# Kernel tuning notes

Measured on AMD Instinct MI355X. Metric: run time of the kernel, lower is better.

## Reference

```python
import jax, jax.numpy as jnp
import numpy as np

B, R, NM, H, P1, G1, RC1, LAT = 16384, 360, 200, 256, 512, 256, 256, 128


def _linear_params(k, out_f, in_f):
    s = 1.0 / np.sqrt(in_f)
    kw, kb = jax.random.split(k)
    W = jax.random.uniform(kw, (out_f, in_f), minval=-s, maxval=s, dtype=jnp.float32)
    b = jax.random.uniform(kb, (out_f,), minval=-s, maxval=s, dtype=jnp.float32)
    return W, b


def setup_inputs() -> dict:
    key = jax.random.key(0)
    ks = jax.random.split(key, 14)
    x_window = jax.random.normal(ks[0], (B, 3, R), dtype=jnp.float32)
    modes = jax.random.normal(ks[1], (R, NM), dtype=jnp.float32)
    mode_coeff = jax.random.normal(ks[2], (B, NM), dtype=jnp.float32)
    W1, b1 = _linear_params(ks[3], H, 3 * R)      # surrogate layer 1
    W2, b2 = _linear_params(ks[4], H, H)          # surrogate layer 2
    W3, b3 = _linear_params(ks[5], R, H)          # surrogate layer 3
    Wp1, bp1 = _linear_params(ks[6], P1, R * R)   # npi_proj
    Wp2, bp2 = _linear_params(ks[7], LAT, P1)
    Wg1, bg1 = _linear_params(ks[8], G1, NM)      # geo_proj
    Wg2, bg2 = _linear_params(ks[9], LAT, G1)
    Wr1, br1 = _linear_params(ks[10], RC1, LAT)   # recon
    Wr2, br2 = _linear_params(ks[11], R, RC1)
    return dict(x_window=x_window, modes=modes, mode_coeff=mode_coeff,
                W1=W1, b1=b1, W2=W2, b2=b2, W3=W3, b3=b3,
                Wp1=Wp1, bp1=bp1, Wp2=Wp2, bp2=bp2,
                Wg1=Wg1, bg1=bg1, Wg2=Wg2, bg2=bg2,
                Wr1=Wr1, br1=br1, Wr2=Wr2, br2=br2)


def reference(x_window, modes, mode_coeff,
              W1, b1, W2, b2, W3, b3,
              Wp1, bp1, Wp2, bp2,
              Wg1, bg1, Wg2, bg2,
              Wr1, br1, Wr2, br2):
    Bs = x_window.shape[0]
    Rr = W3.shape[0]
    # ---- NPI surrogate forward (needed for ReLU masks) ----
    z = x_window.reshape(Bs, 3 * Rr)                       # (B, 3R)
    h1 = z @ W1.T + b1                                     # (B, H)
    m1 = (h1 > 0).astype(z.dtype)
    h2 = (h1 * m1) @ W2.T + b2                             # (B, H)
    m2 = (h2 > 0).astype(z.dtype)
    # ---- EC: exact batch-mean Jacobian of the ReLU MLP w.r.t last timestep ----
    # mean_b [ W3 diag(m2_b) W2 diag(m1_b) W1_last ] = W3 @ (W2 * (m2^T m1 / B)) @ W1[:, -R:]
    G = (m2.T @ m1) / Bs                                   # (H, H)
    ec = W3 @ ((W2 * G) @ W1[:, -Rr:])                     # (R, R); row j = dy_j/dx
    ec = jax.lax.stop_gradient(ec)                         # create_graph=False in original
    # ---- projections ----
    ec_flat = ec.reshape(1, Rr * Rr)
    z_npi1 = jax.nn.relu(ec_flat @ Wp1.T + bp1) @ Wp2.T + bp2   # (1, LAT)
    z_npi = jnp.tile(z_npi1, (Bs, 1))                           # (B, LAT)
    z_geo = jax.nn.relu(mode_coeff @ Wg1.T + bg1) @ Wg2.T + bg2  # (B, LAT)
    zsum = z_npi + z_geo
    zn = zsum / jnp.maximum(jnp.linalg.norm(zsum, axis=-1, keepdims=True), 1e-12)
    recon = jax.nn.relu(zn @ Wr1.T + br1) @ Wr2.T + br2          # (B, R)
    return (z_npi, z_geo, zn, ec, recon)
```

## Files before the change

kernel.cpp:

```cpp
#include <hip/hip_runtime.h>

typedef __bf16 bf16x8 __attribute__((ext_vector_type(8)));
typedef __bf16 bf16x4 __attribute__((ext_vector_type(4)));
typedef float  f32x4  __attribute__((ext_vector_type(4)));

__device__ __forceinline__ f32x4 mfma_bf16(bf16x8 a, bf16x8 b, f32x4 c) {
  return __builtin_amdgcn_mfma_f32_16x16x32_bf16(a, b, c, 0, 0, 0);
}
__device__ __forceinline__ bf16x8 ldB(const __bf16* Bp, int kt, int NT, int nt,
                                      int lane) {
  return *reinterpret_cast<const bf16x8*>(Bp + (((size_t)kt * NT + nt) * 64 + lane) * 8);
}

__device__ __forceinline__ void gridbar(int* cnt, int target) {
  __syncthreads();
  if (threadIdx.x == 0) {
    __threadfence();
    __hip_atomic_fetch_add(cnt, 1, __ATOMIC_RELEASE, __HIP_MEMORY_SCOPE_AGENT);
    while (__hip_atomic_load(cnt, __ATOMIC_RELAXED, __HIP_MEMORY_SCOPE_AGENT) < target)
      __builtin_amdgcn_s_sleep(4);
    __threadfence();
  }
  __syncthreads();
}

__global__ void pack_all(const float* __restrict__ W1, const float* __restrict__ W2,
                         const float* __restrict__ Wg1, const float* __restrict__ Wg2,
                         const float* __restrict__ Wr1, const float* __restrict__ Wr2,
                         __bf16* __restrict__ W1p, __bf16* __restrict__ W2p,
                         __bf16* __restrict__ Wg1p, __bf16* __restrict__ Wg2p,
                         __bf16* __restrict__ Wr1p, __bf16* __restrict__ Wr2p,
                         float* __restrict__ G, int* __restrict__ cnt) {
  int bx = blockIdx.x;
  int lane = threadIdx.x;
  if (bx >= 1104) {
    if (bx == 1104 && lane < 2) cnt[lane] = 0;
    float4* g = (float4*)G;
    int base = (bx - 1104) * 512 + lane;
#pragma unroll
    for (int i = 0; i < 8; ++i) g[base + i * 64] = make_float4(0.f, 0.f, 0.f, 0.f);
    return;
  }
  const float* W; __bf16* out; int N, K, NT, local;
  if (bx < 544)      { W = W1;  out = W1p;  N = 256; K = 1080; NT = 16; local = bx; }
  else if (bx < 672) { W = W2;  out = W2p;  N = 256; K = 256;  NT = 16; local = bx - 544; }
  else if (bx < 784) { W = Wg1; out = Wg1p; N = 256; K = 200;  NT = 16; local = bx - 672; }
  else if (bx < 848) { W = Wg2; out = Wg2p; N = 128; K = 256;  NT = 8;  local = bx - 784; }
  else if (bx < 912) { W = Wr1; out = Wr1p; N = 256; K = 128;  NT = 16; local = bx - 848; }
  else               { W = Wr2; out = Wr2p; N = 360; K = 256;  NT = 24; local = bx - 912; }
  int nt = local % NT, kt = local / NT;
  int n = nt * 16 + (lane & 15);
  int k0 = kt * 32 + (lane >> 4) * 8;
  bf16x8 v;
#pragma unroll
  for (int e = 0; e < 8; ++e) {
    int k = k0 + e;
    float xv = (n < N && k < K) ? W[(size_t)n * K + k] : 0.f;
    v[e] = (__bf16)xv;
  }
  *reinterpret_cast<bf16x8*>(out + ((size_t)local * 64 + lane) * 8) = v;
}

__global__ __launch_bounds__(512) void h1h2_fused(
    const float* __restrict__ x, const __bf16* __restrict__ W1p,
    const float* __restrict__ b1, const __bf16* __restrict__ W2p,
    const float* __restrict__ b2, __bf16* __restrict__ m1T,
    __bf16* __restrict__ m2T) {
  __shared__ __bf16 Alds[32][68];
  __shared__ __bf16 h1s[32][264];
  int tid = threadIdx.x;
  int lane = tid & 63, wid = tid >> 6;
  int wr = wid >> 2, wc = wid & 3;
  int rowBase = blockIdx.x * 32;
  int sr = tid >> 4, sc = (tid & 15) * 4;
  const float* aSrc = x + (size_t)(rowBase + sr) * 1080;
  f32x4 acc[4] = {};
  float4 c0, c1;
  auto LD = [&](int s, float4& d) {
    int gk = s * 64 + sc;
    d = (gk < 1080) ? *(const float4*)(aSrc + gk) : make_float4(0.f, 0.f, 0.f, 0.f);
  };
  LD(0, c0);
  LD(1, c1);
  for (int s = 0; s < 17; ++s) {
    bf16x4 w4;
    w4[0] = (__bf16)c0.x; w4[1] = (__bf16)c0.y;
    w4[2] = (__bf16)c0.z; w4[3] = (__bf16)c0.w;
    *reinterpret_cast<bf16x4*>(&Alds[sr][sc]) = w4;
    __syncthreads();
    c0 = c1;
    if (s + 2 < 17) LD(s + 2, c1);
    int arow = wr * 16 + (lane & 15);
#pragma unroll
    for (int ks = 0; ks < 2; ++ks) {
      int ak = ks * 32 + (lane >> 4) * 8;
      bf16x8 a0 = *reinterpret_cast<const bf16x8*>(&Alds[arow][ak]);
      int kt = s * 2 + ks;
#pragma unroll
      for (int n = 0; n < 4; ++n) {
        bf16x8 bv = ldB(W1p, kt, 16, wc * 4 + n, lane);
        acc[n] = mfma_bf16(a0, bv, acc[n]);
      }
    }
    __syncthreads();
  }
  int q4 = (lane >> 4) * 4;
#pragma unroll
  for (int n = 0; n < 4; ++n) {
    int col = wc * 64 + n * 16 + (lane & 15);
    float bb = b1[col];
#pragma unroll
    for (int j = 0; j < 4; ++j) {
      int rl = wr * 16 + q4 + j;
      float h = acc[n][j] + bb;
      m1T[(size_t)col * 16384 + rowBase + rl] = (__bf16)(h > 0.f ? 1.f : 0.f);
      h1s[rl][col] = (__bf16)fmaxf(h, 0.f);
    }
  }
  __syncthreads();
  f32x4 acc2[4] = {};
#pragma unroll
  for (int ks = 0; ks < 8; ++ks) {
    int arow = wr * 16 + (lane & 15), ak = ks * 32 + (lane >> 4) * 8;
    bf16x8 a0 = *reinterpret_cast<const bf16x8*>(&h1s[arow][ak]);
#pragma unroll
    for (int n = 0; n < 4; ++n) {
      bf16x8 bv = ldB(W2p, ks, 16, wc * 4 + n, lane);
      acc2[n] = mfma_bf16(a0, bv, acc2[n]);
    }
  }
#pragma unroll
  for (int n = 0; n < 4; ++n) {
    int col = wc * 64 + n * 16 + (lane & 15);
    float bb = b2[col];
#pragma unroll
    for (int j = 0; j < 4; ++j) {
      int rl = wr * 16 + q4 + j;
      float h = acc2[n][j] + bb;
      m2T[(size_t)col * 16384 + rowBase + rl] = (__bf16)(h > 0.f ? 1.f : 0.f);
    }
  }
}

__global__ __launch_bounds__(256) void gemm_masks(
    const __bf16* __restrict__ m2T, const __bf16* __restrict__ m1T,
    float* __restrict__ G) {
  int tid = threadIdx.x;
  int lane = tid & 63, wid = tid >> 6;
  int wr = wid >> 1, wc = wid & 1;
  int ibase = blockIdx.x * 64, jbase = blockIdx.y * 64;
  size_t b0 = (size_t)blockIdx.z * 1024 + (lane >> 4) * 8;
  const __bf16* pa0 = m2T + (size_t)(ibase + wr * 32 + (lane & 15)) * 16384 + b0;
  const __bf16* pa1 = pa0 + (size_t)16 * 16384;
  const __bf16* pb0 = m1T + (size_t)(jbase + wc * 32 + (lane & 15)) * 16384 + b0;
  const __bf16* pb1 = pb0 + (size_t)16 * 16384;
  f32x4 acc[2][2] = {};
#pragma unroll 4
  for (int c = 0; c < 32; ++c) {
    bf16x8 a0 = *reinterpret_cast<const bf16x8*>(pa0 + c * 32);
    bf16x8 a1 = *reinterpret_cast<const bf16x8*>(pa1 + c * 32);
    bf16x8 bv0 = *reinterpret_cast<const bf16x8*>(pb0 + c * 32);
    bf16x8 bv1 = *reinterpret_cast<const bf16x8*>(pb1 + c * 32);
    acc[0][0] = mfma_bf16(a0, bv0, acc[0][0]);
    acc[0][1] = mfma_bf16(a0, bv1, acc[0][1]);
    acc[1][0] = mfma_bf16(a1, bv0, acc[1][0]);
    acc[1][1] = mfma_bf16(a1, bv1, acc[1][1]);
  }
  int q4 = (lane >> 4) * 4;
#pragma unroll
  for (int m = 0; m < 2; ++m)
#pragma unroll
    for (int n = 0; n < 2; ++n)
#pragma unroll
      for (int j = 0; j < 4; ++j) {
        int gi = ibase + wr * 32 + m * 16 + q4 + j;
        int gj = jbase + wc * 32 + n * 16 + (lane & 15);
        atomicAdd(&G[(size_t)gi * 256 + gj], acc[m][n][j] * (1.f / 16384.f));
      }
}

__device__ void small_body2(float (*As)[17], float (*Bs)[65], int t,
                            const float* __restrict__ A, const float* __restrict__ A2,
                            int lda, const float* __restrict__ Bm, int ldb,
                            bool sum4, size_t bStride, float* __restrict__ C,
                            int ldc, int M, int N, int kBeg, int kEnd,
                            int m0, int n0) {
  int tx = t & 15, ty = t >> 4;
  float acc[4][4] = {};
  for (int k0 = kBeg; k0 < kEnd; k0 += 16) {
#pragma unroll
    for (int i = 0; i < 4; ++i) {
      int idx = t * 4 + i;
      int r = idx >> 4, kk = idx & 15;
      int gm = m0 + r, gk = k0 + kk;
      float v = (gm < M) ? A[(size_t)gm * lda + gk] : 0.f;
      if (A2 && gm < M) v *= A2[(size_t)gm * lda + gk];
      As[r][kk] = v;
      int kk2 = idx >> 6, cc = idx & 63;
      int gk2 = k0 + kk2, gn = n0 + cc;
      float bv = 0.f;
      if (gn < N) {
        const float* bp = Bm + (size_t)gk2 * ldb + gn;
        bv = bp[0];
        if (sum4) bv = bv + bp[bStride] + bp[2 * bStride] + bp[3 * bStride];
      }
      Bs[kk2][cc] = bv;
    }
    __syncthreads();
#pragma unroll
    for (int kk = 0; kk < 16; ++kk)
#pragma unroll
      for (int i = 0; i < 4; ++i)
#pragma unroll
        for (int j = 0; j < 4; ++j)
          acc[i][j] += As[ty * 4 + i][kk] * Bs[kk][tx * 4 + j];
    __syncthreads();
  }
#pragma unroll
  for (int i = 0; i < 4; ++i)
#pragma unroll
    for (int j = 0; j < 4; ++j) {
      int gm = m0 + ty * 4 + i, gn = n0 + tx * 4 + j;
      if (gm < M && gn < N) C[(size_t)gm * ldc + gn] = acc[i][j];
    }
}

__global__ __launch_bounds__(256) void small_split(
    const float* __restrict__ W2, const float* __restrict__ G,
    const float* __restrict__ W1, const float* __restrict__ W3,
    float* __restrict__ Tpart, float* __restrict__ ecpart,
    float* __restrict__ o_ec, int* __restrict__ cnt) {
  __shared__ float As[64][17];
  __shared__ float Bs[16][65];
  int t = threadIdx.x, bid = blockIdx.x;
  if (bid < 96) {
    int tile = bid >> 2, kc = bid & 3;
    small_body2(As, Bs, t, W2, G, 256, W1 + 720, 1080, false, 0,
                Tpart + (size_t)kc * 98304, 384, 256, 360,
                kc * 64, kc * 64 + 64, (tile / 6) * 64, (tile % 6) * 64);
  }
  gridbar(cnt, 144);
  {
    int tile = bid >> 2, kc = bid & 3;
    small_body2(As, Bs, t, W3, nullptr, 256, Tpart, 384, true, 98304,
                ecpart + (size_t)kc * 129600, 360, 360, 360,
                kc * 64, kc * 64 + 64, (tile / 6) * 64, (tile % 6) * 64);
  }
  gridbar(cnt, 288);
  {
    int base = bid * 900;
    for (int i = t; i < 900; i += 256) {
      int idx = base + i;
      o_ec[idx] = ecpart[idx] + ecpart[129600 + idx] + ecpart[259200 + idx] +
                  ecpart[388800 + idx];
    }
  }
}

__global__ __launch_bounds__(512) void p_and_g1(
    const float* __restrict__ Wp1, const float* __restrict__ ec,
    float* __restrict__ pPart,
    const float* __restrict__ mc, const __bf16* __restrict__ Wg1p,
    const float* __restrict__ bg1, const __bf16* __restrict__ Wg2p,
    const float* __restrict__ bg2, float* __restrict__ o_zgeo) {
  __shared__ __align__(16) char SM[39424];
  int t = threadIdx.x;
  if (blockIdx.x < 256) {
    int lane = t & 63, w = t >> 6;
    int task = blockIdx.x * 8 + w;
    int row = task >> 2;
    int seg = task & 3;
    const float4* wseg = (const float4*)(Wp1 + (size_t)row * 129600) + seg * 8100;
    const float4* eseg = (const float4*)ec + seg * 8100;
    float s = 0.f;
#pragma unroll 4
    for (int i = lane; i < 8100; i += 64) {
      float4 a = wseg[i], b = eseg[i];
      s += a.x * b.x + a.y * b.y + a.z * b.z + a.w * b.w;
    }
    for (int o = 32; o; o >>= 1) s += __shfl_down(s, o);
    if (lane == 0) pPart[seg * 512 + row] = s;
  } else {
    __bf16 (*Alds)[40] = (__bf16(*)[40])SM;
    __bf16 (*g1S)[264] = (__bf16(*)[264])(SM + 5120);
    int lane = t & 63, wid = t >> 6;
    int wr = wid >> 2, wc = wid & 3;
    int rowBase = (blockIdx.x - 256) * 64;
    int sr = t >> 3, sc = (t & 7) * 4;
    const float* aSrc = mc + (size_t)(rowBase + sr) * 200;
    int q4 = (lane >> 4) * 4;
    f32x4 acc[2][4] = {};
    for (int kt = 0; kt < 7; ++kt) {
      int gk = kt * 32 + sc;
      bf16x4 w4;
      if (gk < 200) {
        float4 v = *(const float4*)(aSrc + gk);
        w4[0] = (__bf16)v.x; w4[1] = (__bf16)v.y;
        w4[2] = (__bf16)v.z; w4[3] = (__bf16)v.w;
      } else {
        w4[0] = w4[1] = w4[2] = w4[3] = (__bf16)0.f;
      }
      *reinterpret_cast<bf16x4*>(&Alds[sr][sc]) = w4;
      __syncthreads();
      int arow = wr * 32 + (lane & 15), ak = (lane >> 4) * 8;
      bf16x8 a0 = *reinterpret_cast<const bf16x8*>(&Alds[arow][ak]);
      bf16x8 a1 = *reinterpret_cast<const bf16x8*>(&Alds[arow + 16][ak]);
#pragma unroll
      for (int n = 0; n < 4; ++n) {
        bf16x8 bv = ldB(Wg1p, kt, 16, wc * 4 + n, lane);
        acc[0][n] = mfma_bf16(a0, bv, acc[0][n]);
        acc[1][n] = mfma_bf16(a1, bv, acc[1][n]);
      }
      __syncthreads();
    }
#pragma unroll
    for (int m = 0; m < 2; ++m)
#pragma unroll
      for (int n = 0; n < 4; ++n) {
        int col = wc * 64 + n * 16 + (lane & 15);
        float bb = bg1[col];
#pragma unroll
        for (int j = 0; j < 4; ++j) {
          int rl = wr * 32 + m * 16 + q4 + j;
          g1S[rl][col] = (__bf16)fmaxf(acc[m][n][j] + bb, 0.f);
        }
      }
    __syncthreads();
    f32x4 acc2[2][2] = {};
#pragma unroll
    for (int ks = 0; ks < 8; ++ks) {
      int arow = wr * 32 + (lane & 15), ak = ks * 32 + (lane >> 4) * 8;
      bf16x8 a0 = *reinterpret_cast<const bf16x8*>(&g1S[arow][ak]);
      bf16x8 a1 = *reinterpret_cast<const bf16x8*>(&g1S[arow + 16][ak]);
#pragma unroll
      for (int n = 0; n < 2; ++n) {
        bf16x8 bv = ldB(Wg2p, ks, 8, wc * 2 + n, lane);
        acc2[0][n] = mfma_bf16(a0, bv, acc2[0][n]);
        acc2[1][n] = mfma_bf16(a1, bv, acc2[1][n]);
      }
    }
#pragma unroll
    for (int m = 0; m < 2; ++m)
#pragma unroll
      for (int n = 0; n < 2; ++n) {
        int col = wc * 32 + n * 16 + (lane & 15);
        float bb = bg2[col];
#pragma unroll
        for (int j = 0; j < 4; ++j) {
          int row = rowBase + wr * 32 + m * 16 + q4 + j;
          o_zgeo[(size_t)row * 128 + col] = acc2[m][n][j] + bb;
        }
      }
  }
}

__global__ void gemv_z(const float* __restrict__ pPart,
                       const float* __restrict__ bp1,
                       const float* __restrict__ Wp2,
                       const float* __restrict__ bp2,
                       float* __restrict__ znpi1) {
  __shared__ __align__(16) float pS[512];
  int j = blockIdx.x;
  int t = threadIdx.x;
#pragma unroll
  for (int r0 = 0; r0 < 512; r0 += 64) {
    int r = r0 + t;
    float v = pPart[r] + pPart[512 + r] + pPart[1024 + r] + pPart[1536 + r];
    pS[r] = fmaxf(v + bp1[r], 0.f);
  }
  __syncthreads();
  const float4* w = (const float4*)(Wp2 + (size_t)j * 512);
  const float4* pp = (const float4*)pS;
  float4 a0 = w[t], b0 = pp[t];
  float4 a1 = w[t + 64], b1 = pp[t + 64];
  float s = a0.x * b0.x + a0.y * b0.y + a0.z * b0.z + a0.w * b0.w +
            a1.x * b1.x + a1.y * b1.y + a1.z * b1.z + a1.w * b1.w;
  for (int o = 32; o; o >>= 1) s += __shfl_down(s, o);
  if (t == 0) znpi1[j] = s + bp2[j];
}

__global__ __launch_bounds__(512) void mega_tail(
    const float* __restrict__ zgeo, const float* __restrict__ znpi1,
    const __bf16* __restrict__ Wr1p, const float* __restrict__ br1,
    const __bf16* __restrict__ Wr2p, const float* __restrict__ br2,
    float* __restrict__ o_znpi, float* __restrict__ o_zn,
    float* __restrict__ o_rec) {
  __shared__ __bf16 r1S[64][264];
  __shared__ __bf16 znS[64][136];
  __shared__ float znpiS[128];
  int tid = threadIdx.x;
  int lane = tid & 63, wid = tid >> 6;
  int wr = wid >> 2, wc = wid & 3;
  int rowBase = blockIdx.x * 64;
  int q4 = (lane >> 4) * 4;
  if (tid < 128) znpiS[tid] = znpi1[tid];
  __syncthreads();
  {
    int rg = tid >> 5;
    int c4 = (tid & 31) * 4;
    float4 zp = make_float4(znpiS[c4], znpiS[c4 + 1], znpiS[c4 + 2], znpiS[c4 + 3]);
#pragma unroll
    for (int ri = 0; ri < 4; ++ri) {
      int rl = rg + ri * 16;
      int row = rowBase + rl;
      float4 zg = *(const float4*)(zgeo + (size_t)row * 128 + c4);
      float4 zs = make_float4(zg.x + zp.x, zg.y + zp.y, zg.z + zp.z, zg.w + zp.w);
      *(float4*)(o_znpi + (size_t)row * 128 + c4) = zp;
      float ss = zs.x * zs.x + zs.y * zs.y + zs.z * zs.z + zs.w * zs.w;
      ss += __shfl_xor(ss, 1);
      ss += __shfl_xor(ss, 2);
      ss += __shfl_xor(ss, 4);
      ss += __shfl_xor(ss, 8);
      ss += __shfl_xor(ss, 16);
      float rn = 1.f / fmaxf(sqrtf(ss), 1e-12f);
      float4 zn = make_float4(zs.x * rn, zs.y * rn, zs.z * rn, zs.w * rn);
      *(float4*)(o_zn + (size_t)row * 128 + c4) = zn;
      bf16x4 znb;
      znb[0] = (__bf16)zn.x; znb[1] = (__bf16)zn.y;
      znb[2] = (__bf16)zn.z; znb[3] = (__bf16)zn.w;
      *reinterpret_cast<bf16x4*>(&znS[rl][c4]) = znb;
    }
  }
  __syncthreads();
  {
    f32x4 acc[2][4] = {};
#pragma unroll
    for (int ks = 0; ks < 4; ++ks) {
      int arow = wr * 32 + (lane & 15), ak = ks * 32 + (lane >> 4) * 8;
      bf16x8 a0 = *reinterpret_cast<const bf16x8*>(&znS[arow][ak]);
      bf16x8 a1 = *reinterpret_cast<const bf16x8*>(&znS[arow + 16][ak]);
#pragma unroll
      for (int n = 0; n < 4; ++n) {
        bf16x8 bv = ldB(Wr1p, ks, 16, wc * 4 + n, lane);
        acc[0][n] = mfma_bf16(a0, bv, acc[0][n]);
        acc[1][n] = mfma_bf16(a1, bv, acc[1][n]);
      }
    }
#pragma unroll
    for (int m = 0; m < 2; ++m)
#pragma unroll
      for (int n = 0; n < 4; ++n) {
        int col = wc * 64 + n * 16 + (lane & 15);
        float bb = br1[col];
#pragma unroll
        for (int j = 0; j < 4; ++j) {
          int rl = wr * 32 + m * 16 + q4 + j;
          r1S[rl][col] = (__bf16)fmaxf(acc[m][n][j] + bb, 0.f);
        }
      }
  }
  __syncthreads();
  {
    f32x4 acc[2][6] = {};
#pragma unroll
    for (int ks = 0; ks < 8; ++ks) {
      int arow = wr * 32 + (lane & 15), ak = ks * 32 + (lane >> 4) * 8;
      bf16x8 a0 = *reinterpret_cast<const bf16x8*>(&r1S[arow][ak]);
      bf16x8 a1 = *reinterpret_cast<const bf16x8*>(&r1S[arow + 16][ak]);
#pragma unroll
      for (int n = 0; n < 6; ++n) {
        bf16x8 bv = ldB(Wr2p, ks, 24, wc * 6 + n, lane);
        acc[0][n] = mfma_bf16(a0, bv, acc[0][n]);
        acc[1][n] = mfma_bf16(a1, bv, acc[1][n]);
      }
    }
#pragma unroll
    for (int m = 0; m < 2; ++m)
#pragma unroll
      for (int n = 0; n < 6; ++n) {
        int col = wc * 96 + n * 16 + (lane & 15);
        if (col < 360) {
          float bb = br2[col];
#pragma unroll
          for (int j = 0; j < 4; ++j) {
            int rl = wr * 32 + m * 16 + q4 + j;
            o_rec[(size_t)(rowBase + rl) * 360 + col] = acc[m][n][j] + bb;
          }
        }
      }
  }
}

extern "C" void kernel_launch(void* const* d_in, const int* in_sizes, int n_in,
                              void* d_out, int out_size, void* d_ws,
                              size_t ws_size, hipStream_t stream) {
  (void)in_sizes; (void)n_in; (void)out_size; (void)ws_size;
  const float* x   = (const float*)d_in[0];
  const float* mc  = (const float*)d_in[2];
  const float* W1  = (const float*)d_in[3];  const float* b1  = (const float*)d_in[4];
  const float* W2  = (const float*)d_in[5];  const float* b2  = (const float*)d_in[6];
  const float* W3  = (const float*)d_in[7];
  const float* Wp1 = (const float*)d_in[9];  const float* bp1 = (const float*)d_in[10];
  const float* Wp2 = (const float*)d_in[11]; const float* bp2 = (const float*)d_in[12];
  const float* Wg1 = (const float*)d_in[13]; const float* bg1 = (const float*)d_in[14];
  const float* Wg2 = (const float*)d_in[15]; const float* bg2 = (const float*)d_in[16];
  const float* Wr1 = (const float*)d_in[17]; const float* br1 = (const float*)d_in[18];
  const float* Wr2 = (const float*)d_in[19]; const float* br2 = (const float*)d_in[20];

  float* out = (float*)d_out;
  float* o_znpi = out;
  float* o_zgeo = out + 2097152;
  float* o_zn   = out + 4194304;
  float* o_ec   = out + 6291456;
  float* o_rec  = out + 6421056;

  char* ws = (char*)d_ws;
  __bf16* m1T    = (__bf16*)(ws + 0);
  __bf16* m2T    = (__bf16*)(ws + 8388608);
  float*  G      = (float*)(ws + 16777216);
  float*  Tpart  = (float*)(ws + 17039360);
  float*  ecpart = (float*)(ws + 18612224);
  float*  pPart  = (float*)(ws + 20686848);
  float*  znpi1  = (float*)(ws + 20695040);
  __bf16* W1p    = (__bf16*)(ws + 20695552);
  __bf16* W2p    = W1p  + (size_t)544 * 512;
  __bf16* Wg1p   = W2p  + (size_t)128 * 512;
  __bf16* Wg2p   = Wg1p + (size_t)112 * 512;
  __bf16* Wr1p   = Wg2p + (size_t)64 * 512;
  __bf16* Wr2p   = Wr1p + (size_t)64 * 512;
  int*    cnt    = (int*)(ws + 22020096);

  pack_all<<<1136, 64, 0, stream>>>(W1, W2, Wg1, Wg2, Wr1, Wr2,
                                    W1p, W2p, Wg1p, Wg2p, Wr1p, Wr2p, G, cnt);
  h1h2_fused<<<512, 512, 0, stream>>>(x, W1p, b1, W2p, b2, m1T, m2T);
  gemm_masks<<<dim3(4, 4, 16), 256, 0, stream>>>(m2T, m1T, G);
  small_split<<<144, 256, 0, stream>>>(W2, G, W1, W3, Tpart, ecpart, o_ec,
                                       cnt);
  p_and_g1<<<512, 512, 0, stream>>>(Wp1, o_ec, pPart, mc, Wg1p, bg1,
                                    Wg2p, bg2, o_zgeo);
  gemv_z<<<128, 64, 0, stream>>>(pPart, bp1, Wp2, bp2, znpi1);
  mega_tail<<<256, 512, 0, stream>>>(o_zgeo, znpi1, Wr1p, br1, Wr2p, br2,
                                     o_znpi, o_zn, o_rec);
}
```

Before: 225.1 us.

## Co-schedule geo projection with mask GEMM, fold z_npi gemv into tail kernel

The geo projection (mode_coeff through Wg1/Wg2) moves out of the Wp1 GEMV kernel and runs in the same launch as the mask Gram GEMM, so independent work overlaps with it. The Wp1 GEMV becomes its own kernel with one row per block and 8 segments per row. The small Wp2 GEMV that produces z_npi is recomputed inside every mega_tail block instead of running as a separate launch. This removes one kernel launch and the dependency stall, at the cost of the Wp2 GEMV being repeated in all 256 tail blocks and half-idle 512-thread blocks in the mask part.

```diff
diff --git a/kernel.cpp b/kernel.cpp
--- a/kernel.cpp
+++ b/kernel.cpp
@@ -34,7 +34,7 @@
   int bx = blockIdx.x;
   int lane = threadIdx.x;
   if (bx >= 1104) {
-    if (bx == 1104 && lane < 2) cnt[lane] = 0;
+    if (bx == 1104 && lane == 0) cnt[0] = 0;
     float4* g = (float4*)G;
     int base = (bx - 1104) * 512 + lane;
 #pragma unroll
@@ -142,41 +142,120 @@
   }
 }
 
-__global__ __launch_bounds__(256) void gemm_masks(
+__global__ __launch_bounds__(512) void masks_g1(
     const __bf16* __restrict__ m2T, const __bf16* __restrict__ m1T,
-    float* __restrict__ G) {
-  int tid = threadIdx.x;
-  int lane = tid & 63, wid = tid >> 6;
-  int wr = wid >> 1, wc = wid & 1;
-  int ibase = blockIdx.x * 64, jbase = blockIdx.y * 64;
-  size_t b0 = (size_t)blockIdx.z * 1024 + (lane >> 4) * 8;
-  const __bf16* pa0 = m2T + (size_t)(ibase + wr * 32 + (lane & 15)) * 16384 + b0;
-  const __bf16* pa1 = pa0 + (size_t)16 * 16384;
-  const __bf16* pb0 = m1T + (size_t)(jbase + wc * 32 + (lane & 15)) * 16384 + b0;
-  const __bf16* pb1 = pb0 + (size_t)16 * 16384;
-  f32x4 acc[2][2] = {};
+    float* __restrict__ G,
+    const float* __restrict__ mc, const __bf16* __restrict__ Wg1p,
+    const float* __restrict__ bg1, const __bf16* __restrict__ Wg2p,
+    const float* __restrict__ bg2, float* __restrict__ o_zgeo) {
+  __shared__ __align__(16) char SM[39424];
+  int tid = threadIdx.x, bid = blockIdx.x;
+  if (bid < 256) {
+    if (tid >= 256) return;
+    int lane = tid & 63, wid = tid >> 6;
+    int wr = wid >> 1, wc = wid & 1;
+    int i = (bid >> 2) & 3, j = bid & 3, z = bid >> 4;
+    int ibase = i * 64, jbase = j * 64;
+    size_t b0 = (size_t)z * 1024 + (lane >> 4) * 8;
+    const __bf16* pa0 = m2T + (size_t)(ibase + wr * 32 + (lane & 15)) * 16384 + b0;
+    const __bf16* pa1 = pa0 + (size_t)16 * 16384;
+    const __bf16* pb0 = m1T + (size_t)(jbase + wc * 32 + (lane & 15)) * 16384 + b0;
+    const __bf16* pb1 = pb0 + (size_t)16 * 16384;
+    f32x4 acc[2][2] = {};
 #pragma unroll 4
-  for (int c = 0; c < 32; ++c) {
-    bf16x8 a0 = *reinterpret_cast<const bf16x8*>(pa0 + c * 32);
-    bf16x8 a1 = *reinterpret_cast<const bf16x8*>(pa1 + c * 32);
-    bf16x8 bv0 = *reinterpret_cast<const bf16x8*>(pb0 + c * 32);
-    bf16x8 bv1 = *reinterpret_cast<const bf16x8*>(pb1 + c * 32);
-    acc[0][0] = mfma_bf16(a0, bv0, acc[0][0]);
-    acc[0][1] = mfma_bf16(a0, bv1, acc[0][1]);
-    acc[1][0] = mfma_bf16(a1, bv0, acc[1][0]);
-    acc[1][1] = mfma_bf16(a1, bv1, acc[1][1]);
-  }
-  int q4 = (lane >> 4) * 4;
-#pragma unroll
-  for (int m = 0; m < 2; ++m)
-#pragma unroll
-    for (int n = 0; n < 2; ++n)
-#pragma unroll
-      for (int j = 0; j < 4; ++j) {
-        int gi = ibase + wr * 32 + m * 16 + q4 + j;
-        int gj = jbase + wc * 32 + n * 16 + (lane & 15);
-        atomicAdd(&G[(size_t)gi * 256 + gj], acc[m][n][j] * (1.f / 16384.f));
-      }
+    for (int c = 0; c < 32; ++c) {
+      bf16x8 a0 = *reinterpret_cast<const bf16x8*>(pa0 + c * 32);
+      bf16x8 a1 = *reinterpret_cast<const bf16x8*>(pa1 + c * 32);
+      bf16x8 bv0 = *reinterpret_cast<const bf16x8*>(pb0 + c * 32);
+      bf16x8 bv1 = *reinterpret_cast<const bf16x8*>(pb1 + c * 32);
+      acc[0][0] = mfma_bf16(a0, bv0, acc[0][0]);
+      acc[0][1] = mfma_bf16(a0, bv1, acc[0][1]);
+      acc[1][0] = mfma_bf16(a1, bv0, acc[1][0]);
+      acc[1][1] = mfma_bf16(a1, bv1, acc[1][1]);
+    }
+    int q4 = (lane >> 4) * 4;
+#pragma unroll
+    for (int m = 0; m < 2; ++m)
+#pragma unroll
+      for (int n = 0; n < 2; ++n)
+#pragma unroll
+        for (int jj = 0; jj < 4; ++jj) {
+          int gi = ibase + wr * 32 + m * 16 + q4 + jj;
+          int gj = jbase + wc * 32 + n * 16 + (lane & 15);
+          atomicAdd(&G[(size_t)gi * 256 + gj], acc[m][n][jj] * (1.f / 16384.f));
+        }
+  } else {
+    __bf16 (*Alds)[40] = (__bf16(*)[40])SM;
+    __bf16 (*g1S)[264] = (__bf16(*)[264])(SM + 5120);
+    int lane = tid & 63, wid = tid >> 6;
+    int wr = wid >> 2, wc = wid & 3;
+    int rowBase = (bid - 256) * 64;
+    int sr = tid >> 3, sc = (tid & 7) * 4;
+    const float* aSrc = mc + (size_t)(rowBase + sr) * 200;
+    int q4 = (lane >> 4) * 4;
+    f32x4 acc[2][4] = {};
+    for (int kt = 0; kt < 7; ++kt) {
+      int gk = kt * 32 + sc;
+      bf16x4 w4;
+      if (gk < 200) {
+        float4 v = *(const float4*)(aSrc + gk);
+        w4[0] = (__bf16)v.x; w4[1] = (__bf16)v.y;
+        w4[2] = (__bf16)v.z; w4[3] = (__bf16)v.w;
+      } else {
+        w4[0] = w4[1] = w4[2] = w4[3] = (__bf16)0.f;
+      }
+      *reinterpret_cast<bf16x4*>(&Alds[sr][sc]) = w4;
+      __syncthreads();
+      int arow = wr * 32 + (lane & 15), ak = (lane >> 4) * 8;
+      bf16x8 a0 = *reinterpret_cast<const bf16x8*>(&Alds[arow][ak]);
+      bf16x8 a1 = *reinterpret_cast<const bf16x8*>(&Alds[arow + 16][ak]);
+#pragma unroll
+      for (int n = 0; n < 4; ++n) {
+        bf16x8 bv = ldB(Wg1p, kt, 16, wc * 4 + n, lane);
+        acc[0][n] = mfma_bf16(a0, bv, acc[0][n]);
+        acc[1][n] = mfma_bf16(a1, bv, acc[1][n]);
+      }
+      __syncthreads();
+    }
+#pragma unroll
+    for (int m = 0; m < 2; ++m)
+#pragma unroll
+      for (int n = 0; n < 4; ++n) {
+        int col = wc * 64 + n * 16 + (lane & 15);
+        float bb = bg1[col];
+#pragma unroll
+        for (int j = 0; j < 4; ++j) {
+          int rl = wr * 32 + m * 16 + q4 + j;
+          g1S[rl][col] = (__bf16)fmaxf(acc[m][n][j] + bb, 0.f);
+        }
+      }
+    __syncthreads();
+    f32x4 acc2[2][2] = {};
+#pragma unroll
+    for (int ks = 0; ks < 8; ++ks) {
+      int arow = wr * 32 + (lane & 15), ak = ks * 32 + (lane >> 4) * 8;
+      bf16x8 a0 = *reinterpret_cast<const bf16x8*>(&g1S[arow][ak]);
+      bf16x8 a1 = *reinterpret_cast<const bf16x8*>(&g1S[arow + 16][ak]);
+#pragma unroll
+      for (int n = 0; n < 2; ++n) {
+        bf16x8 bv = ldB(Wg2p, ks, 8, wc * 2 + n, lane);
+        acc2[0][n] = mfma_bf16(a0, bv, acc2[0][n]);
+        acc2[1][n] = mfma_bf16(a1, bv, acc2[1][n]);
+      }
+    }
+#pragma unroll
+    for (int m = 0; m < 2; ++m)
+#pragma unroll
+      for (int n = 0; n < 2; ++n) {
+        int col = wc * 32 + n * 16 + (lane & 15);
+        float bb = bg2[col];
+#pragma unroll
+        for (int j = 0; j < 4; ++j) {
+          int row = rowBase + wr * 32 + m * 16 + q4 + j;
+          o_zgeo[(size_t)row * 128 + col] = acc2[m][n][j] + bb;
+        }
+      }
+  }
 }
 
 __device__ void small_body2(float (*As)[17], float (*Bs)[65], int t,
@@ -257,130 +336,28 @@
   }
 }
 
-__global__ __launch_bounds__(512) void p_and_g1(
+__global__ __launch_bounds__(512) void p_gemv(
     const float* __restrict__ Wp1, const float* __restrict__ ec,
-    float* __restrict__ pPart,
-    const float* __restrict__ mc, const __bf16* __restrict__ Wg1p,
-    const float* __restrict__ bg1, const __bf16* __restrict__ Wg2p,
-    const float* __restrict__ bg2, float* __restrict__ o_zgeo) {
-  __shared__ __align__(16) char SM[39424];
+    float* __restrict__ pPart) {
   int t = threadIdx.x;
-  if (blockIdx.x < 256) {
-    int lane = t & 63, w = t >> 6;
-    int task = blockIdx.x * 8 + w;
-    int row = task >> 2;
-    int seg = task & 3;
-    const float4* wseg = (const float4*)(Wp1 + (size_t)row * 129600) + seg * 8100;
-    const float4* eseg = (const float4*)ec + seg * 8100;
-    float s = 0.f;
+  int lane = t & 63, seg = t >> 6;
+  int row = blockIdx.x;
+  const float4* wseg = (const float4*)(Wp1 + (size_t)row * 129600) + seg * 4050;
+  const float4* eseg = (const float4*)ec + seg * 4050;
+  float s = 0.f;
 #pragma unroll 4
-    for (int i = lane; i < 8100; i += 64) {
-      float4 a = wseg[i], b = eseg[i];
-      s += a.x * b.x + a.y * b.y + a.z * b.z + a.w * b.w;
-    }
-    for (int o = 32; o; o >>= 1) s += __shfl_down(s, o);
-    if (lane == 0) pPart[seg * 512 + row] = s;
-  } else {
-    __bf16 (*Alds)[40] = (__bf16(*)[40])SM;
-    __bf16 (*g1S)[264] = (__bf16(*)[264])(SM + 5120);
-    int lane = t & 63, wid = t >> 6;
-    int wr = wid >> 2, wc = wid & 3;
-    int rowBase = (blockIdx.x - 256) * 64;
-    int sr = t >> 3, sc = (t & 7) * 4;
-    const float* aSrc = mc + (size_t)(rowBase + sr) * 200;
-    int q4 = (lane >> 4) * 4;
-    f32x4 acc[2][4] = {};
-    for (int kt = 0; kt < 7; ++kt) {
-      int gk = kt * 32 + sc;
-      bf16x4 w4;
-      if (gk < 200) {
-        float4 v = *(const float4*)(aSrc + gk);
-        w4[0] = (__bf16)v.x; w4[1] = (__bf16)v.y;
-        w4[2] = (__bf16)v.z; w4[3] = (__bf16)v.w;
-      } else {
-        w4[0] = w4[1] = w4[2] = w4[3] = (__bf16)0.f;
-      }
-      *reinterpret_cast<bf16x4*>(&Alds[sr][sc]) = w4;
-      __syncthreads();
-      int arow = wr * 32 + (lane & 15), ak = (lane >> 4) * 8;
-      bf16x8 a0 = *reinterpret_cast<const bf16x8*>(&Alds[arow][ak]);
-      bf16x8 a1 = *reinterpret_cast<const bf16x8*>(&Alds[arow + 16][ak]);
-#pragma unroll
-      for (int n = 0; n < 4; ++n) {
-        bf16x8 bv = ldB(Wg1p, kt, 16, wc * 4 + n, lane);
-        acc[0][n] = mfma_bf16(a0, bv, acc[0][n]);
-        acc[1][n] = mfma_bf16(a1, bv, acc[1][n]);
-      }
-      __syncthreads();
-    }
-#pragma unroll
-    for (int m = 0; m < 2; ++m)
-#pragma unroll
-      for (int n = 0; n < 4; ++n) {
-        int col = wc * 64 + n * 16 + (lane & 15);
-        float bb = bg1[col];
-#pragma unroll
-        for (int j = 0; j < 4; ++j) {
-          int rl = wr * 32 + m * 16 + q4 + j;
-          g1S[rl][col] = (__bf16)fmaxf(acc[m][n][j] + bb, 0.f);
-        }
-      }
-    __syncthreads();
-    f32x4 acc2[2][2] = {};
-#pragma unroll
-    for (int ks = 0; ks < 8; ++ks) {
-      int arow = wr * 32 + (lane & 15), ak = ks * 32 + (lane >> 4) * 8;
-      bf16x8 a0 = *reinterpret_cast<const bf16x8*>(&g1S[arow][ak]);
-      bf16x8 a1 = *reinterpret_cast<const bf16x8*>(&g1S[arow + 16][ak]);
-#pragma unroll
-      for (int n = 0; n < 2; ++n) {
-        bf16x8 bv = ldB(Wg2p, ks, 8, wc * 2 + n, lane);
-        acc2[0][n] = mfma_bf16(a0, bv, acc2[0][n]);
-        acc2[1][n] = mfma_bf16(a1, bv, acc2[1][n]);
-      }
-    }
-#pragma unroll
-    for (int m = 0; m < 2; ++m)
-#pragma unroll
-      for (int n = 0; n < 2; ++n) {
-        int col = wc * 32 + n * 16 + (lane & 15);
-        float bb = bg2[col];
-#pragma unroll
-        for (int j = 0; j < 4; ++j) {
-          int row = rowBase + wr * 32 + m * 16 + q4 + j;
-          o_zgeo[(size_t)row * 128 + col] = acc2[m][n][j] + bb;
-        }
-      }
-  }
-}
-
-__global__ void gemv_z(const float* __restrict__ pPart,
-                       const float* __restrict__ bp1,
-                       const float* __restrict__ Wp2,
-                       const float* __restrict__ bp2,
-                       float* __restrict__ znpi1) {
-  __shared__ __align__(16) float pS[512];
-  int j = blockIdx.x;
-  int t = threadIdx.x;
-#pragma unroll
-  for (int r0 = 0; r0 < 512; r0 += 64) {
-    int r = r0 + t;
-    float v = pPart[r] + pPart[512 + r] + pPart[1024 + r] + pPart[1536 + r];
-    pS[r] = fmaxf(v + bp1[r], 0.f);
-  }
-  __syncthreads();
-  const float4* w = (const float4*)(Wp2 + (size_t)j * 512);
-  const float4* pp = (const float4*)pS;
-  float4 a0 = w[t], b0 = pp[t];
-  float4 a1 = w[t + 64], b1 = pp[t + 64];
-  float s = a0.x * b0.x + a0.y * b0.y + a0.z * b0.z + a0.w * b0.w +
-            a1.x * b1.x + a1.y * b1.y + a1.z * b1.z + a1.w * b1.w;
+  for (int i = lane; i < 4050; i += 64) {
+    float4 a = wseg[i], b = eseg[i];
+    s += a.x * b.x + a.y * b.y + a.z * b.z + a.w * b.w;
+  }
   for (int o = 32; o; o >>= 1) s += __shfl_down(s, o);
-  if (t == 0) znpi1[j] = s + bp2[j];
+  if (lane == 0) pPart[seg * 512 + row] = s;
 }
 
 __global__ __launch_bounds__(512) void mega_tail(
-    const float* __restrict__ zgeo, const float* __restrict__ znpi1,
+    const float* __restrict__ pPart, const float* __restrict__ bp1,
+    const float* __restrict__ Wp2, const float* __restrict__ bp2,
+    const float* __restrict__ zgeo,
     const __bf16* __restrict__ Wr1p, const float* __restrict__ br1,
     const __bf16* __restrict__ Wr2p, const float* __restrict__ br2,
     float* __restrict__ o_znpi, float* __restrict__ o_zn,
@@ -388,12 +365,33 @@
   __shared__ __bf16 r1S[64][264];
   __shared__ __bf16 znS[64][136];
   __shared__ float znpiS[128];
+  __shared__ __align__(16) float pS[512];
   int tid = threadIdx.x;
   int lane = tid & 63, wid = tid >> 6;
   int wr = wid >> 2, wc = wid & 3;
   int rowBase = blockIdx.x * 64;
   int q4 = (lane >> 4) * 4;
-  if (tid < 128) znpiS[tid] = znpi1[tid];
+  {
+    float v = pPart[tid] + pPart[512 + tid] + pPart[1024 + tid] +
+              pPart[1536 + tid] + pPart[2048 + tid] + pPart[2560 + tid] +
+              pPart[3072 + tid] + pPart[3584 + tid];
+    pS[tid] = fmaxf(v + bp1[tid], 0.f);
+  }
+  __syncthreads();
+  {
+    int col = tid >> 2, q = tid & 3;
+    const float4* w = (const float4*)(Wp2 + (size_t)col * 512 + q * 128);
+    const float4* pv = (const float4*)(pS + q * 128);
+    float s = 0.f;
+#pragma unroll
+    for (int i = 0; i < 32; ++i) {
+      float4 a = w[i], b = pv[i];
+      s += a.x * b.x + a.y * b.y + a.z * b.z + a.w * b.w;
+    }
+    s += __shfl_xor(s, 1);
+    s += __shfl_xor(s, 2);
+    if (q == 0) znpiS[col] = s + bp2[col];
+  }
   __syncthreads();
   {
     int rg = tid >> 5;
@@ -511,8 +509,7 @@
   float*  Tpart  = (float*)(ws + 17039360);
   float*  ecpart = (float*)(ws + 18612224);
   float*  pPart  = (float*)(ws + 20686848);
-  float*  znpi1  = (float*)(ws + 20695040);
-  __bf16* W1p    = (__bf16*)(ws + 20695552);
+  __bf16* W1p    = (__bf16*)(ws + 20703232);
   __bf16* W2p    = W1p  + (size_t)544 * 512;
   __bf16* Wg1p   = W2p  + (size_t)128 * 512;
   __bf16* Wg2p   = Wg1p + (size_t)112 * 512;
@@ -523,12 +520,11 @@
   pack_all<<<1136, 64, 0, stream>>>(W1, W2, Wg1, Wg2, Wr1, Wr2,
                                     W1p, W2p, Wg1p, Wg2p, Wr1p, Wr2p, G, cnt);
   h1h2_fused<<<512, 512, 0, stream>>>(x, W1p, b1, W2p, b2, m1T, m2T);
-  gemm_masks<<<dim3(4, 4, 16), 256, 0, stream>>>(m2T, m1T, G);
+  masks_g1<<<512, 512, 0, stream>>>(m2T, m1T, G, mc, Wg1p, bg1, Wg2p, bg2,
+                                    o_zgeo);
   small_split<<<144, 256, 0, stream>>>(W2, G, W1, W3, Tpart, ecpart, o_ec,
                                        cnt);
-  p_and_g1<<<512, 512, 0, stream>>>(Wp1, o_ec, pPart, mc, Wg1p, bg1,
-                                    Wg2p, bg2, o_zgeo);
-  gemv_z<<<128, 64, 0, stream>>>(pPart, bp1, Wp2, bp2, znpi1);
-  mega_tail<<<256, 512, 0, stream>>>(o_zgeo, znpi1, Wr1p, br1, Wr2p, br2,
-                                     o_znpi, o_zn, o_rec);
-}
+  p_gemv<<<512, 512, 0, stream>>>(Wp1, o_ec, pPart);
+  mega_tail<<<256, 512, 0, stream>>>(pPart, bp1, Wp2, bp2, o_zgeo, Wr1p, br1,
+                                     Wr2p, br2, o_znpi, o_zn, o_rec);
+}
```

New measurement: 229.7 us. +2.0%, slower.
